# Kernel tuning notes

Measured on AMD Instinct MI355X. Metric: run time of the kernel, lower is better.

The kernel has to match this reference:

```python
import jax, jax.numpy as jnp
import numpy as np

EPS = 1e-06


def rotation_trick(e, q):
    # e, q: (..., D). Faithful to torch version, but r_rT @ e and
    # q_hat_e_hatT @ e are algebraically simplified to r*(r.e) and
    # q_hat*(e_hat.e), avoiding the (..., D, D) outer-product tensors.
    sg = jax.lax.stop_gradient
    e_norm = sg(jnp.linalg.norm(e, axis=-1, keepdims=True)) + EPS
    q_norm = sg(jnp.linalg.norm(q, axis=-1, keepdims=True)) + EPS
    e_hat = sg(e / e_norm)
    q_hat = sg(q / q_norm)
    lmbda = q_norm / e_norm
    r = e_hat + q_hat
    r = r / jnp.linalg.norm(r, axis=-1, keepdims=True)
    r_dot_e = jnp.sum(r * e, axis=-1, keepdims=True)
    ehat_dot_e = jnp.sum(e_hat * e, axis=-1, keepdims=True)
    return lmbda * (e - 2.0 * r * r_dot_e + 2.0 * q_hat * ehat_dot_e)


def setup_inputs() -> dict:
    key = jax.random.key(0)
    k1, k2 = jax.random.split(key)
    B, D, H, W = 8, 64, 32, 32
    K = 8192
    x = jax.random.normal(k1, (B, D, H, W), dtype=jnp.float32)
    # init_tensor: L2-normalize uniform rand along dim=1, scale=1
    e = jax.random.uniform(k2, (D, K), dtype=jnp.float32)
    e_i_ts = e / (jnp.linalg.norm(e, axis=1, keepdims=True) + 1e-12)
    return {"x": x, "e_i_ts": e_i_ts}


def reference(x, e_i_ts):
    # x: (B, D, H, W); e_i_ts: (D, K)
    B, D, H, W = x.shape
    x_perm = jnp.transpose(x, (0, 2, 3, 1))          # (B, H, W, D)
    flat_x = x_perm.reshape(-1, D)                   # (N, D)
    distances = (
        jnp.sum(flat_x**2, axis=1, keepdims=True)
        - 2.0 * flat_x @ e_i_ts
        + jnp.sum(e_i_ts**2, axis=0, keepdims=True)
    )                                                # (N, K)
    encoding_indices = jnp.argmin(distances, axis=1) # (N,)
    ind = encoding_indices.reshape(B, H, W)
    quantized_x = e_i_ts.T[ind]                      # (B, H, W, D) gather
    quantized_x_d = rotation_trick(x_perm, quantized_x)
    # permute back to channels-first
    q = jnp.transpose(quantized_x, (0, 3, 1, 2))
    q_d = jnp.transpose(quantized_x_d, (0, 3, 1, 2))
    return (q_d, q, ind)
```

## Files before the change

### kernel.cpp

```cpp
#include <hip/hip_runtime.h>
#include <float.h>
#include <math.h>

#define EPS 1e-6f

typedef __attribute__((ext_vector_type(8))) short short8;
typedef __attribute__((ext_vector_type(4))) float f32x4;

constexpr int Nn = 8192;
constexpr int Dd = 64;
constexpr int Kk = 8192;
constexpr int PLANE = Nn * Dd;
constexpr int KSPLIT = 16;
constexpr int KPB = Kk / KSPLIT;
constexpr int NT = KPB / 16;
constexpr int NPAIR = NT / 2;
constexpr int TILE_USH = 6 * 64 * 8;
constexpr int TILE_BYTES = TILE_USH * 2;

__device__ __forceinline__ void split3(float v, unsigned short& h1, unsigned short& h2, unsigned short& h3) {
    unsigned u = __float_as_uint(v);
    h1 = (unsigned short)(u >> 16);
    float r1 = v - __uint_as_float((unsigned)h1 << 16);
    h2 = (unsigned short)(__float_as_uint(r1) >> 16);
    float r2 = r1 - __uint_as_float((unsigned)h2 << 16);
    h3 = (unsigned short)(__float_as_uint(r2) >> 16);
}

typedef __attribute__((address_space(3))) unsigned int lds_u32_t;
typedef __attribute__((address_space(1))) unsigned int glb_u32_t;
__device__ __forceinline__ void gload_lds16(const void* g, void* l) {
    __builtin_amdgcn_global_load_lds((const glb_u32_t*)g, (lds_u32_t*)l, 16, 0, 0);
}

__global__ void prep_kernel(const float* __restrict__ e, const float* __restrict__ x,
                            unsigned short* __restrict__ es_t, float* __restrict__ en2h,
                            float* __restrict__ et,
                            unsigned short* __restrict__ xs, float* __restrict__ xn2)
{
    const int tid = threadIdx.x;
    if (blockIdx.x < 32) {
        const int k = blockIdx.x * 256 + tid;
        const int t = k >> 4, l15 = k & 15;
        unsigned short* tb = es_t + (size_t)t * TILE_USH;
        float s = 0.f;
        #pragma unroll
        for (int c = 0; c < 8; ++c) {
            const int ks = c >> 2, kg = c & 3;
            short8 h1v, h2v, h3v;
            float fv[8];
            #pragma unroll
            for (int j = 0; j < 8; ++j) {
                float v = e[(c * 8 + j) * Kk + k];
                fv[j] = v;
                s = fmaf(v, v, s);
                unsigned short h1, h2, h3; split3(v, h1, h2, h3);
                h1v[j] = (short)h1; h2v[j] = (short)h2; h3v[j] = (short)h3;
            }
            const int lofs = (kg * 16 + l15) * 8;
            *(short8*)(tb + (0 * 2 + ks) * 512 + lofs) = h1v;
            *(short8*)(tb + (1 * 2 + ks) * 512 + lofs) = h2v;
            *(short8*)(tb + (2 * 2 + ks) * 512 + lofs) = h3v;
            *(float4*)(et + (size_t)k * Dd + c * 8)     = *(float4*)&fv[0];
            *(float4*)(et + (size_t)k * Dd + c * 8 + 4) = *(float4*)&fv[4];
        }
        en2h[k] = 0.5f * s;
    } else {
        const int p = (blockIdx.x - 32) * 256 + tid;
        const int b = p >> 10, hw = p & 1023;
        float s = 0.f;
        #pragma unroll
        for (int c = 0; c < 8; ++c) {
            short8 h1v, h2v, h3v;
            #pragma unroll
            for (int j = 0; j < 8; ++j) {
                float v = x[(b * Dd + c * 8 + j) * 1024 + hw];
                s = fmaf(v, v, s);
                unsigned short h1, h2, h3; split3(-v, h1, h2, h3);
                h1v[j] = (short)h1; h2v[j] = (short)h2; h3v[j] = (short)h3;
            }
            *(short8*)(xs + (size_t)p * Dd + c * 8) = h1v;
            *(short8*)(xs + PLANE + (size_t)p * Dd + c * 8) = h2v;
            *(short8*)(xs + 2 * PLANE + (size_t)p * Dd + c * 8) = h3v;
        }
        xn2[p] = s;
    }
}

__device__ __forceinline__ void tile_compute(
    const short8 (&a)[2][3][2], const short8 (&b)[6], float en,
    int nb, int l15, float (&bv)[2][4], int (&bi)[2][4])
{
    f32x4 acc[2][2];
    acc[0][0] = f32x4{en, en, en, en}; acc[1][0] = f32x4{en, en, en, en};
    acc[0][1] = f32x4{0.f, 0.f, 0.f, 0.f}; acc[1][1] = f32x4{0.f, 0.f, 0.f, 0.f};
    #define PROD(sx, se) \
        acc[0][0] = __builtin_amdgcn_mfma_f32_16x16x32_bf16(a[0][sx][0], b[(se)*2+0], acc[0][0], 0,0,0); \
        acc[1][0] = __builtin_amdgcn_mfma_f32_16x16x32_bf16(a[1][sx][0], b[(se)*2+0], acc[1][0], 0,0,0); \
        acc[0][1] = __builtin_amdgcn_mfma_f32_16x16x32_bf16(a[0][sx][1], b[(se)*2+1], acc[0][1], 0,0,0); \
        acc[1][1] = __builtin_amdgcn_mfma_f32_16x16x32_bf16(a[1][sx][1], b[(se)*2+1], acc[1][1], 0,0,0);
    PROD(0,0) PROD(0,1) PROD(1,0) PROD(0,2) PROD(1,1) PROD(2,0)
    #undef PROD
    #pragma unroll
    for (int mi = 0; mi < 2; ++mi)
        #pragma unroll
        for (int j = 0; j < 4; ++j) {
            float s = acc[mi][0][j] + acc[mi][1][j];
            if (s < bv[mi][j]) { bv[mi][j] = s; bi[mi][j] = nb + l15; }
        }
}

__global__ __launch_bounds__(256, 2) void dist_mfma(
    const unsigned short* __restrict__ xs, const unsigned short* __restrict__ es_t,
    const float* __restrict__ en2h,
    float* __restrict__ pval, int* __restrict__ pidx)
{
    __shared__ __align__(16) unsigned short sB[2][2 * TILE_USH];

    const int tid = threadIdx.x;
    const int w = tid >> 6, lane = tid & 63;
    const int l15 = lane & 15, kg = lane >> 4;
    const int m0 = blockIdx.x * 128 + w * 32;
    const int t0 = blockIdx.y * NT;

    short8 a[2][3][2];
    #pragma unroll
    for (int mi = 0; mi < 2; ++mi) {
        const unsigned short* xp = xs + (size_t)(m0 + mi * 16 + l15) * Dd + kg * 8;
        #pragma unroll
        for (int s = 0; s < 3; ++s)
            #pragma unroll
            for (int ks = 0; ks < 2; ++ks)
                a[mi][s][ks] = *(const short8*)(xp + s * PLANE + ks * 32);
    }

    float bv[2][4]; int bi[2][4];
    #pragma unroll
    for (int mi = 0; mi < 2; ++mi)
        #pragma unroll
        for (int j = 0; j < 4; ++j) { bv[mi][j] = FLT_MAX; bi[mi][j] = 0; }

    #define STAGE_PAIR(buf, pi) { \
        const char* gb_ = (const char*)es_t + (size_t)(pi) * (2 * TILE_BYTES); \
        char* lb_ = (char*)&sB[buf][0]; \
        _Pragma("unroll") \
        for (int r_ = 0; r_ < 3; ++r_) { \
            const int off_ = r_ * 4096 + w * 1024; \
            gload_lds16(gb_ + off_ + lane * 16, lb_ + off_); } }

    STAGE_PAIR(0, t0 / 2)
    __syncthreads();

    #pragma unroll 1
    for (int p = 0; p < NPAIR; ++p) {
        const int cur = p & 1;
        if (p + 1 < NPAIR) { STAGE_PAIR(cur ^ 1, t0 / 2 + p + 1) }

        const int ti = t0 + p * 2;
        float en0 = en2h[ti * 16 + l15];
        float en1 = en2h[ti * 16 + 16 + l15];

        short8 bf0[6], bf1[6];
        {
            const unsigned short* lb = &sB[cur][lane * 8];
            #pragma unroll
            for (int f = 0; f < 6; ++f) bf0[f] = *(const short8*)(lb + f * 512);
            #pragma unroll
            for (int f = 0; f < 6; ++f) bf1[f] = *(const short8*)(lb + TILE_USH + f * 512);
        }
        tile_compute(a, bf0, en0, ti * 16, l15, bv, bi);
        tile_compute(a, bf1, en1, ti * 16 + 16, l15, bv, bi);

        __syncthreads();
    }

    #pragma unroll
    for (int m = 1; m < 16; m <<= 1) {
        #pragma unroll
        for (int mi = 0; mi < 2; ++mi)
            #pragma unroll
            for (int j = 0; j < 4; ++j) {
                float ov = __shfl_xor(bv[mi][j], m, 64);
                int   oi = __shfl_xor(bi[mi][j], m, 64);
                if (ov < bv[mi][j] || (ov == bv[mi][j] && oi < bi[mi][j])) {
                    bv[mi][j] = ov; bi[mi][j] = oi;
                }
            }
    }
    if (l15 == 0) {
        #pragma unroll
        for (int mi = 0; mi < 2; ++mi)
            #pragma unroll
            for (int j = 0; j < 4; ++j) {
                int pix = m0 + mi * 16 + kg * 4 + j;
                pval[(size_t)pix * KSPLIT + blockIdx.y] = bv[mi][j];
                pidx[(size_t)pix * KSPLIT + blockIdx.y] = bi[mi][j];
            }
    }
}

__global__ __launch_bounds__(256) void finalize_kernel(
    const float* __restrict__ x, const float* __restrict__ et,
    const float* __restrict__ en2h, const float* __restrict__ xn2,
    const float* __restrict__ pval, const int* __restrict__ pidx,
    float* __restrict__ out_qd, float* __restrict__ out_q, float* __restrict__ out_ind)
{
    const int tid = threadIdx.x;
    const int p = blockIdx.x * 256 + tid;

    const float4* pv4 = (const float4*)(pval + (size_t)p * KSPLIT);
    const int4*   pi4 = (const int4*)(pidx + (size_t)p * KSPLIT);
    float bvv = FLT_MAX; int bii = 0;
    #pragma unroll
    for (int u = 0; u < KSPLIT / 4; ++u) {
        float4 v4 = pv4[u]; int4 i4 = pi4[u];
        #pragma unroll
        for (int jj = 0; jj < 4; ++jj) {
            float v = ((const float*)&v4)[jj];
            int   i = ((const int*)&i4)[jj];
            if (v < bvv || (v == bvv && i < bii)) { bvv = v; bii = i; }
        }
    }
    if (blockIdx.y == 0) out_ind[p] = (float)bii;

    float sx2 = xn2[p];
    float enh = en2h[bii];
    float sq2 = 2.f * enh;
    float sxq = enh - bvv;
    float ne = sqrtf(sx2), nq = sqrtf(sq2);
    float inv_e = 1.f / (ne + EPS), inv_q = 1.f / (nq + EPS);
    float lmbda = (nq + EPS) * inv_e;
    float ehat_dot_e = sx2 * inv_e;
    float rn2 = sx2 * inv_e * inv_e + 2.f * sxq * inv_e * inv_q + sq2 * inv_q * inv_q;
    float inv_r = rsqrtf(rn2);
    float rde = (sx2 * inv_e + sxq * inv_q) * inv_r;
    float cx = lmbda * (1.f - 2.f * rde * inv_r * inv_e);
    float cq = 2.f * lmbda * inv_q * (ehat_dot_e - rde * inv_r);

    const int b = p >> 10, hw = p & 1023;
    const int d0 = blockIdx.y * 8;
    const float* xb = x + (b * Dd + d0) * 1024 + hw;
    const float* er = et + (size_t)bii * Dd + d0;
    float* qd_b = out_qd + (b * Dd + d0) * 1024 + hw;
    float* q_b  = out_q  + (b * Dd + d0) * 1024 + hw;
    #pragma unroll
    for (int dv = 0; dv < 2; ++dv) {
        float4 q4 = *(const float4*)(er + dv * 4);
        #pragma unroll
        for (int jj = 0; jj < 4; ++jj) {
            int d = dv * 4 + jj;
            float xv = xb[d * 1024];
            float qv = ((const float*)&q4)[jj];
            qd_b[d * 1024] = cx * xv + cq * qv;
            q_b[d * 1024]  = qv;
        }
    }
}

extern "C" void kernel_launch(void* const* d_in, const int* in_sizes, int n_in,
                              void* d_out, int out_size, void* d_ws, size_t ws_size,
                              hipStream_t stream) {
    const float* x = (const float*)d_in[0];
    const float* e = (const float*)d_in[1];
    float* out = (float*)d_out;
    float* out_qd  = out;
    float* out_q   = out + Nn * Dd;
    float* out_ind = out + 2 * Nn * Dd;

    unsigned short* xs   = (unsigned short*)d_ws;
    unsigned short* es_t = xs + 3 * PLANE;
    float* et   = (float*)(es_t + (size_t)(Kk / 16) * TILE_USH);
    float* en2h = et + (size_t)Kk * Dd;
    float* xn2  = en2h + Kk;
    float* pval = xn2 + Nn;
    int*   pidx = (int*)(pval + (size_t)Nn * KSPLIT);

    prep_kernel<<<64, 256, 0, stream>>>(e, x, es_t, en2h, et, xs, xn2);
    dist_mfma<<<dim3(Nn / 128, KSPLIT), 256, 0, stream>>>(xs, es_t, en2h, pval, pidx);
    finalize_kernel<<<dim3(32, 8), 256, 0, stream>>>(x, et, en2h, xn2, pval, pidx,
                                                     out_qd, out_q, out_ind);
}
```

Before: 64.29 us.

## Software-pipeline codebook LDS staging with explicit vmcnt waits and ping-pong unroll

Restructures the distance kernel's main loop into an unrolled two-stage ping-pong over the two LDS buffers. The next tile pair is staged, along with its norm values, before the current pair is computed. Explicit s_waitcnt vmcnt(5) and raw s_barrier calls replace __syncthreads, so only the older loads are waited on and the prefetch overlaps the MFMA work. The en2h loads are also hoisted one stage ahead. In exchange, the code relies on exact counting of outstanding memory ops and on hand-placed scheduling barriers, and the final iterations issue a redundant clamped prefetch.

```diff
diff --git a/kernel.cpp b/kernel.cpp
--- a/kernel.cpp
+++ b/kernel.cpp
@@ -122,6 +122,7 @@
     const int l15 = lane & 15, kg = lane >> 4;
     const int m0 = blockIdx.x * 128 + w * 32;
     const int t0 = blockIdx.y * NT;
+    const int pr0 = t0 / 2;
 
     short8 a[2][3][2];
     #pragma unroll
@@ -148,30 +149,53 @@
             const int off_ = r_ * 4096 + w * 1024; \
             gload_lds16(gb_ + off_ + lane * 16, lb_ + off_); } }
 
-    STAGE_PAIR(0, t0 / 2)
-    __syncthreads();
+    #define COMPUTE_PAIR(buf, pp_, e0_, e1_) { \
+        const int ti_ = t0 + (pp_) * 2; \
+        short8 bf0[6], bf1[6]; \
+        const unsigned short* lb = &sB[buf][lane * 8]; \
+        _Pragma("unroll") \
+        for (int f = 0; f < 6; ++f) bf0[f] = *(const short8*)(lb + f * 512); \
+        _Pragma("unroll") \
+        for (int f = 0; f < 6; ++f) bf1[f] = *(const short8*)(lb + TILE_USH + f * 512); \
+        tile_compute(a, bf0, e0_, ti_ * 16, l15, bv, bi); \
+        tile_compute(a, bf1, e1_, ti_ * 16 + 16, l15, bv, bi); }
+
+    STAGE_PAIR(0, pr0)
+    float enA0 = en2h[t0 * 16 + l15];
+    float enA1 = en2h[t0 * 16 + 16 + l15];
+    float enB0, enB1;
+    asm volatile("s_waitcnt vmcnt(0)" ::: "memory");
+    __builtin_amdgcn_s_barrier();
+    __builtin_amdgcn_sched_barrier(0);
 
     #pragma unroll 1
-    for (int p = 0; p < NPAIR; ++p) {
-        const int cur = p & 1;
-        if (p + 1 < NPAIR) { STAGE_PAIR(cur ^ 1, t0 / 2 + p + 1) }
-
-        const int ti = t0 + p * 2;
-        float en0 = en2h[ti * 16 + l15];
-        float en1 = en2h[ti * 16 + 16 + l15];
-
-        short8 bf0[6], bf1[6];
+    for (int pp = 0; pp < NPAIR; pp += 2) {
         {
-            const unsigned short* lb = &sB[cur][lane * 8];
-            #pragma unroll
-            for (int f = 0; f < 6; ++f) bf0[f] = *(const short8*)(lb + f * 512);
-            #pragma unroll
-            for (int f = 0; f < 6; ++f) bf1[f] = *(const short8*)(lb + TILE_USH + f * 512);
-        }
-        tile_compute(a, bf0, en0, ti * 16, l15, bv, bi);
-        tile_compute(a, bf1, en1, ti * 16 + 16, l15, bv, bi);
-
-        __syncthreads();
+            const int pn = (pp + 1 < NPAIR) ? pp + 1 : NPAIR - 1;
+            STAGE_PAIR(1, pr0 + pn)
+            enB0 = en2h[(t0 + 2 * pn) * 16 + l15];
+            enB1 = en2h[(t0 + 2 * pn) * 16 + 16 + l15];
+            asm volatile("s_waitcnt vmcnt(5)" ::: "memory");
+            __builtin_amdgcn_sched_barrier(0);
+            __builtin_amdgcn_s_barrier();
+            __builtin_amdgcn_sched_barrier(0);
+            COMPUTE_PAIR(0, pp, enA0, enA1)
+            __builtin_amdgcn_sched_barrier(0);
+            __builtin_amdgcn_s_barrier();
+        }
+        {
+            const int pn = (pp + 2 < NPAIR) ? pp + 2 : NPAIR - 1;
+            STAGE_PAIR(0, pr0 + pn)
+            enA0 = en2h[(t0 + 2 * pn) * 16 + l15];
+            enA1 = en2h[(t0 + 2 * pn) * 16 + 16 + l15];
+            asm volatile("s_waitcnt vmcnt(5)" ::: "memory");
+            __builtin_amdgcn_sched_barrier(0);
+            __builtin_amdgcn_s_barrier();
+            __builtin_amdgcn_sched_barrier(0);
+            COMPUTE_PAIR(1, pp + 1, enB0, enB1)
+            __builtin_amdgcn_sched_barrier(0);
+            __builtin_amdgcn_s_barrier();
+        }
     }
 
     #pragma unroll
```

Result: slower. 66.93 us (+4.1%).

## Fold codeword norms into staged tiles via MFMA and restructure LDS pipeline barriers

Applied to the files above, without the earlier changes.

The half squared norm of each codeword is now split into three bf16 parts and stored as a seventh fragment in each staged tile. A ones-vector MFMA adds it into the accumulator, which removes the per-iteration global loads of en2h. The double-buffered LDS loop now uses explicit s_waitcnt/s_barrier asm: it issues the next prefetch unconditionally, waits only on the older loads, and puts a barrier after the fragment reads instead of at the end of the loop. This adds one MFMA and more LDS traffic per tile, and relies on the hand-written waitcnt counts being correct.

```diff
diff --git a/kernel.cpp b/kernel.cpp
--- a/kernel.cpp
+++ b/kernel.cpp
@@ -15,8 +15,8 @@
 constexpr int KPB = Kk / KSPLIT;
 constexpr int NT = KPB / 16;
 constexpr int NPAIR = NT / 2;
-constexpr int TILE_USH = 6 * 64 * 8;
-constexpr int TILE_BYTES = TILE_USH * 2;
+constexpr int TILE_USH = 4096;
+constexpr int PAIR_BYTES = 2 * TILE_USH * 2;
 
 __device__ __forceinline__ void split3(float v, unsigned short& h1, unsigned short& h2, unsigned short& h3) {
     unsigned u = __float_as_uint(v);
@@ -64,6 +64,13 @@
             *(float4*)(et + (size_t)k * Dd + c * 8)     = *(float4*)&fv[0];
             *(float4*)(et + (size_t)k * Dd + c * 8 + 4) = *(float4*)&fv[4];
         }
+        unsigned short s1, s2, s3; split3(0.5f * s, s1, s2, s3);
+        short8 env = {(short)s1, (short)s2, (short)s3, 0, 0, 0, 0, 0};
+        short8 zz  = {0, 0, 0, 0, 0, 0, 0, 0};
+        *(short8*)(tb + 6 * 512 + l15 * 8) = env;
+        *(short8*)(tb + 6 * 512 + (16 + l15) * 8) = zz;
+        *(short8*)(tb + 6 * 512 + (32 + l15) * 8) = zz;
+        *(short8*)(tb + 6 * 512 + (48 + l15) * 8) = zz;
         en2h[k] = 0.5f * s;
     } else {
         const int p = (blockIdx.x - 32) * 256 + tid;
@@ -88,12 +95,14 @@
 }
 
 __device__ __forceinline__ void tile_compute(
-    const short8 (&a)[2][3][2], const short8 (&b)[6], float en,
+    const short8 (&a)[2][3][2], const short8 a_ones, const short8 (&b)[7],
     int nb, int l15, float (&bv)[2][4], int (&bi)[2][4])
 {
+    const f32x4 zero = {0.f, 0.f, 0.f, 0.f};
+    f32x4 acc_en = __builtin_amdgcn_mfma_f32_16x16x32_bf16(a_ones, b[6], zero, 0, 0, 0);
     f32x4 acc[2][2];
-    acc[0][0] = f32x4{en, en, en, en}; acc[1][0] = f32x4{en, en, en, en};
-    acc[0][1] = f32x4{0.f, 0.f, 0.f, 0.f}; acc[1][1] = f32x4{0.f, 0.f, 0.f, 0.f};
+    acc[0][0] = acc_en; acc[1][0] = acc_en;
+    acc[0][1] = zero;   acc[1][1] = zero;
     #define PROD(sx, se) \
         acc[0][0] = __builtin_amdgcn_mfma_f32_16x16x32_bf16(a[0][sx][0], b[(se)*2+0], acc[0][0], 0,0,0); \
         acc[1][0] = __builtin_amdgcn_mfma_f32_16x16x32_bf16(a[1][sx][0], b[(se)*2+0], acc[1][0], 0,0,0); \
@@ -112,7 +121,6 @@
 
 __global__ __launch_bounds__(256, 2) void dist_mfma(
     const unsigned short* __restrict__ xs, const unsigned short* __restrict__ es_t,
-    const float* __restrict__ en2h,
     float* __restrict__ pval, int* __restrict__ pidx)
 {
     __shared__ __align__(16) unsigned short sB[2][2 * TILE_USH];
@@ -122,6 +130,7 @@
     const int l15 = lane & 15, kg = lane >> 4;
     const int m0 = blockIdx.x * 128 + w * 32;
     const int t0 = blockIdx.y * NT;
+    const int pr0 = t0 / 2;
 
     short8 a[2][3][2];
     #pragma unroll
@@ -133,6 +142,9 @@
             for (int ks = 0; ks < 2; ++ks)
                 a[mi][s][ks] = *(const short8*)(xp + s * PLANE + ks * 32);
     }
+    const short8 a_ones = (kg == 0)
+        ? short8{(short)0x3F80, (short)0x3F80, (short)0x3F80, 0, 0, 0, 0, 0}
+        : short8{0, 0, 0, 0, 0, 0, 0, 0};
 
     float bv[2][4]; int bi[2][4];
     #pragma unroll
@@ -141,37 +153,37 @@
         for (int j = 0; j < 4; ++j) { bv[mi][j] = FLT_MAX; bi[mi][j] = 0; }
 
     #define STAGE_PAIR(buf, pi) { \
-        const char* gb_ = (const char*)es_t + (size_t)(pi) * (2 * TILE_BYTES); \
+        const char* gb_ = (const char*)es_t + (size_t)(pi) * PAIR_BYTES; \
         char* lb_ = (char*)&sB[buf][0]; \
         _Pragma("unroll") \
-        for (int r_ = 0; r_ < 3; ++r_) { \
+        for (int r_ = 0; r_ < 4; ++r_) { \
             const int off_ = r_ * 4096 + w * 1024; \
             gload_lds16(gb_ + off_ + lane * 16, lb_ + off_); } }
 
-    STAGE_PAIR(0, t0 / 2)
-    __syncthreads();
+    STAGE_PAIR(0, pr0)
+    asm volatile("s_waitcnt vmcnt(0)" ::: "memory");
+    asm volatile("s_barrier" ::: "memory");
 
     #pragma unroll 1
-    for (int p = 0; p < NPAIR; ++p) {
-        const int cur = p & 1;
-        if (p + 1 < NPAIR) { STAGE_PAIR(cur ^ 1, t0 / 2 + p + 1) }
-
-        const int ti = t0 + p * 2;
-        float en0 = en2h[ti * 16 + l15];
-        float en1 = en2h[ti * 16 + 16 + l15];
-
-        short8 bf0[6], bf1[6];
-        {
-            const unsigned short* lb = &sB[cur][lane * 8];
-            #pragma unroll
-            for (int f = 0; f < 6; ++f) bf0[f] = *(const short8*)(lb + f * 512);
-            #pragma unroll
-            for (int f = 0; f < 6; ++f) bf1[f] = *(const short8*)(lb + TILE_USH + f * 512);
-        }
-        tile_compute(a, bf0, en0, ti * 16, l15, bv, bi);
-        tile_compute(a, bf1, en1, ti * 16 + 16, l15, bv, bi);
-
-        __syncthreads();
+    for (int pp = 0; pp < NPAIR; ++pp) {
+        const int cur = pp & 1;
+        const int pn = (pp + 1 < NPAIR) ? pp + 1 : NPAIR - 1;
+        STAGE_PAIR(cur ^ 1, pr0 + pn)
+        asm volatile("s_waitcnt vmcnt(4)" ::: "memory");
+        asm volatile("s_barrier" ::: "memory");
+
+        short8 bf0[7], bf1[7];
+        const unsigned short* lb = &sB[cur][lane * 8];
+        #pragma unroll
+        for (int f = 0; f < 7; ++f) bf0[f] = *(const short8*)(lb + f * 512);
+        #pragma unroll
+        for (int f = 0; f < 7; ++f) bf1[f] = *(const short8*)(lb + TILE_USH + f * 512);
+        asm volatile("s_waitcnt lgkmcnt(0)" ::: "memory");
+        asm volatile("s_barrier" ::: "memory");
+
+        const int ti = t0 + pp * 2;
+        tile_compute(a, a_ones, bf0, ti * 16, l15, bv, bi);
+        tile_compute(a, a_ones, bf1, ti * 16 + 16, l15, bv, bi);
     }
 
     #pragma unroll
@@ -276,7 +288,7 @@
     int*   pidx = (int*)(pval + (size_t)Nn * KSPLIT);
 
     prep_kernel<<<64, 256, 0, stream>>>(e, x, es_t, en2h, et, xs, xn2);
-    dist_mfma<<<dim3(Nn / 128, KSPLIT), 256, 0, stream>>>(xs, es_t, en2h, pval, pidx);
+    dist_mfma<<<dim3(Nn / 128, KSPLIT), 256, 0, stream>>>(xs, es_t, pval, pidx);
     finalize_kernel<<<dim3(32, 8), 256, 0, stream>>>(x, et, en2h, xn2, pval, pidx,
                                                      out_qd, out_q, out_ind);
 }
```

Result: no change. 65.44 us (+1.8%).

## Switch distance GEMM to 32x32x16 MFMA with explicit waitcnt double buffering

Applied to the files above, without the earlier changes.

Replaces the 16x16x32 bf16 MFMA tiles with 32x32x16 MFMAs, repacking the codebook tiles in the prep kernel so each LDS tile holds 32 codewords. Each wave now covers 32 pixels by 32 codewords per tile with fewer instructions and less operand traffic per FLOP. The pipeline uses manual s_waitcnt/s_barrier double buffering and setprio around the MFMA block instead of __syncthreads, and the argmin reduction now spans 32 lanes. This costs more accumulator registers and relies on the hand-written wait counts being correct.

```diff
diff --git a/kernel.cpp b/kernel.cpp
--- a/kernel.cpp
+++ b/kernel.cpp
@@ -6,6 +6,7 @@
 
 typedef __attribute__((ext_vector_type(8))) short short8;
 typedef __attribute__((ext_vector_type(4))) float f32x4;
+typedef __attribute__((ext_vector_type(16))) float f32x16;
 
 constexpr int Nn = 8192;
 constexpr int Dd = 64;
@@ -13,9 +14,8 @@
 constexpr int PLANE = Nn * Dd;
 constexpr int KSPLIT = 16;
 constexpr int KPB = Kk / KSPLIT;
-constexpr int NT = KPB / 16;
-constexpr int NPAIR = NT / 2;
-constexpr int TILE_USH = 6 * 64 * 8;
+constexpr int NTILE = KPB / 32;
+constexpr int TILE_USH = 12 * 512;
 constexpr int TILE_BYTES = TILE_USH * 2;
 
 __device__ __forceinline__ void split3(float v, unsigned short& h1, unsigned short& h2, unsigned short& h3) {
@@ -41,12 +41,12 @@
     const int tid = threadIdx.x;
     if (blockIdx.x < 32) {
         const int k = blockIdx.x * 256 + tid;
-        const int t = k >> 4, l15 = k & 15;
+        const int t = k >> 5, cwin = k & 31;
         unsigned short* tb = es_t + (size_t)t * TILE_USH;
         float s = 0.f;
         #pragma unroll
         for (int c = 0; c < 8; ++c) {
-            const int ks = c >> 2, kg = c & 3;
+            const int q = c >> 1, half = c & 1;
             short8 h1v, h2v, h3v;
             float fv[8];
             #pragma unroll
@@ -57,10 +57,10 @@
                 unsigned short h1, h2, h3; split3(v, h1, h2, h3);
                 h1v[j] = (short)h1; h2v[j] = (short)h2; h3v[j] = (short)h3;
             }
-            const int lofs = (kg * 16 + l15) * 8;
-            *(short8*)(tb + (0 * 2 + ks) * 512 + lofs) = h1v;
-            *(short8*)(tb + (1 * 2 + ks) * 512 + lofs) = h2v;
-            *(short8*)(tb + (2 * 2 + ks) * 512 + lofs) = h3v;
+            const int lofs = (cwin + 32 * half) * 8;
+            *(short8*)(tb + (0 * 4 + q) * 512 + lofs) = h1v;
+            *(short8*)(tb + (1 * 4 + q) * 512 + lofs) = h2v;
+            *(short8*)(tb + (2 * 4 + q) * 512 + lofs) = h3v;
             *(float4*)(et + (size_t)k * Dd + c * 8)     = *(float4*)&fv[0];
             *(float4*)(et + (size_t)k * Dd + c * 8 + 4) = *(float4*)&fv[4];
         }
@@ -87,27 +87,28 @@
     }
 }
 
-__device__ __forceinline__ void tile_compute(
-    const short8 (&a)[2][3][2], const short8 (&b)[6], float en,
-    int nb, int l15, float (&bv)[2][4], int (&bi)[2][4])
-{
-    f32x4 acc[2][2];
-    acc[0][0] = f32x4{en, en, en, en}; acc[1][0] = f32x4{en, en, en, en};
-    acc[0][1] = f32x4{0.f, 0.f, 0.f, 0.f}; acc[1][1] = f32x4{0.f, 0.f, 0.f, 0.f};
-    #define PROD(sx, se) \
-        acc[0][0] = __builtin_amdgcn_mfma_f32_16x16x32_bf16(a[0][sx][0], b[(se)*2+0], acc[0][0], 0,0,0); \
-        acc[1][0] = __builtin_amdgcn_mfma_f32_16x16x32_bf16(a[1][sx][0], b[(se)*2+0], acc[1][0], 0,0,0); \
-        acc[0][1] = __builtin_amdgcn_mfma_f32_16x16x32_bf16(a[0][sx][1], b[(se)*2+1], acc[0][1], 0,0,0); \
-        acc[1][1] = __builtin_amdgcn_mfma_f32_16x16x32_bf16(a[1][sx][1], b[(se)*2+1], acc[1][1], 0,0,0);
-    PROD(0,0) PROD(0,1) PROD(1,0) PROD(0,2) PROD(1,1) PROD(2,0)
-    #undef PROD
-    #pragma unroll
-    for (int mi = 0; mi < 2; ++mi)
-        #pragma unroll
-        for (int j = 0; j < 4; ++j) {
-            float s = acc[mi][0][j] + acc[mi][1][j];
-            if (s < bv[mi][j]) { bv[mi][j] = s; bi[mi][j] = nb + l15; }
-        }
+__device__ __forceinline__ void tile_compute32(
+    const short8 (&a)[3][4], const short8 (&b)[12], float en,
+    int cw, float (&bv)[16], int (&bi)[16])
+{
+    f32x16 acc0, acc1;
+    #pragma unroll
+    for (int r = 0; r < 16; ++r) { acc0[r] = en; acc1[r] = 0.f; }
+    #define PRODQ(q) { \
+        f32x16& ac = ((q) & 1) ? acc1 : acc0; \
+        ac = __builtin_amdgcn_mfma_f32_32x32x16_bf16(a[0][q], b[0 * 4 + (q)], ac, 0,0,0); \
+        ac = __builtin_amdgcn_mfma_f32_32x32x16_bf16(a[0][q], b[1 * 4 + (q)], ac, 0,0,0); \
+        ac = __builtin_amdgcn_mfma_f32_32x32x16_bf16(a[1][q], b[0 * 4 + (q)], ac, 0,0,0); \
+        ac = __builtin_amdgcn_mfma_f32_32x32x16_bf16(a[0][q], b[2 * 4 + (q)], ac, 0,0,0); \
+        ac = __builtin_amdgcn_mfma_f32_32x32x16_bf16(a[1][q], b[1 * 4 + (q)], ac, 0,0,0); \
+        ac = __builtin_amdgcn_mfma_f32_32x32x16_bf16(a[2][q], b[0 * 4 + (q)], ac, 0,0,0); }
+    PRODQ(0) PRODQ(1) PRODQ(2) PRODQ(3)
+    #undef PRODQ
+    #pragma unroll
+    for (int r = 0; r < 16; ++r) {
+        float v = acc0[r] + acc1[r];
+        if (v < bv[r]) { bv[r] = v; bi[r] = cw; }
+    }
 }
 
 __global__ __launch_bounds__(256, 2) void dist_mfma(
@@ -115,87 +116,93 @@
     const float* __restrict__ en2h,
     float* __restrict__ pval, int* __restrict__ pidx)
 {
-    __shared__ __align__(16) unsigned short sB[2][2 * TILE_USH];
+    __shared__ __align__(16) unsigned short sB[2][TILE_USH];
 
     const int tid = threadIdx.x;
     const int w = tid >> 6, lane = tid & 63;
-    const int l15 = lane & 15, kg = lane >> 4;
+    const int col = lane & 31, half = lane >> 5;
     const int m0 = blockIdx.x * 128 + w * 32;
-    const int t0 = blockIdx.y * NT;
-
-    short8 a[2][3][2];
-    #pragma unroll
-    for (int mi = 0; mi < 2; ++mi) {
-        const unsigned short* xp = xs + (size_t)(m0 + mi * 16 + l15) * Dd + kg * 8;
-        #pragma unroll
-        for (int s = 0; s < 3; ++s)
-            #pragma unroll
-            for (int ks = 0; ks < 2; ++ks)
-                a[mi][s][ks] = *(const short8*)(xp + s * PLANE + ks * 32);
-    }
-
-    float bv[2][4]; int bi[2][4];
-    #pragma unroll
-    for (int mi = 0; mi < 2; ++mi)
-        #pragma unroll
-        for (int j = 0; j < 4; ++j) { bv[mi][j] = FLT_MAX; bi[mi][j] = 0; }
-
-    #define STAGE_PAIR(buf, pi) { \
-        const char* gb_ = (const char*)es_t + (size_t)(pi) * (2 * TILE_BYTES); \
+    const int tg0 = blockIdx.y * NTILE;
+    const int k0 = blockIdx.y * KPB;
+
+    short8 a[3][4];
+    #pragma unroll
+    for (int s = 0; s < 3; ++s)
+        #pragma unroll
+        for (int q = 0; q < 4; ++q)
+            a[s][q] = *(const short8*)(xs + (size_t)(m0 + col) * Dd + s * PLANE + q * 16 + 8 * half);
+
+    float bv[16]; int bi[16];
+    #pragma unroll
+    for (int r = 0; r < 16; ++r) { bv[r] = FLT_MAX; bi[r] = 0; }
+
+    #define STAGE_TILE(buf, ti) { \
+        const char* gb_ = (const char*)es_t + (size_t)(tg0 + (ti)) * TILE_BYTES; \
         char* lb_ = (char*)&sB[buf][0]; \
         _Pragma("unroll") \
         for (int r_ = 0; r_ < 3; ++r_) { \
             const int off_ = r_ * 4096 + w * 1024; \
             gload_lds16(gb_ + off_ + lane * 16, lb_ + off_); } }
 
-    STAGE_PAIR(0, t0 / 2)
-    __syncthreads();
+    #define DSREAD(bf, buf) { \
+        const unsigned short* lb = &sB[buf][lane * 8]; \
+        _Pragma("unroll") \
+        for (int f = 0; f < 12; ++f) bf[f] = *(const short8*)(lb + f * 512); }
+
+    STAGE_TILE(0, 0)
+    float enA = en2h[k0 + col];
+    float enB;
+    asm volatile("s_waitcnt vmcnt(0)" ::: "memory");
+    asm volatile("s_barrier" ::: "memory");
 
     #pragma unroll 1
-    for (int p = 0; p < NPAIR; ++p) {
-        const int cur = p & 1;
-        if (p + 1 < NPAIR) { STAGE_PAIR(cur ^ 1, t0 / 2 + p + 1) }
-
-        const int ti = t0 + p * 2;
-        float en0 = en2h[ti * 16 + l15];
-        float en1 = en2h[ti * 16 + 16 + l15];
-
-        short8 bf0[6], bf1[6];
+    for (int tt = 0; tt < NTILE; tt += 2) {
         {
-            const unsigned short* lb = &sB[cur][lane * 8];
-            #pragma unroll
-            for (int f = 0; f < 6; ++f) bf0[f] = *(const short8*)(lb + f * 512);
-            #pragma unroll
-            for (int f = 0; f < 6; ++f) bf1[f] = *(const short8*)(lb + TILE_USH + f * 512);
-        }
-        tile_compute(a, bf0, en0, ti * 16, l15, bv, bi);
-        tile_compute(a, bf1, en1, ti * 16 + 16, l15, bv, bi);
-
-        __syncthreads();
-    }
-
-    #pragma unroll
-    for (int m = 1; m < 16; m <<= 1) {
-        #pragma unroll
-        for (int mi = 0; mi < 2; ++mi)
-            #pragma unroll
-            for (int j = 0; j < 4; ++j) {
-                float ov = __shfl_xor(bv[mi][j], m, 64);
-                int   oi = __shfl_xor(bi[mi][j], m, 64);
-                if (ov < bv[mi][j] || (ov == bv[mi][j] && oi < bi[mi][j])) {
-                    bv[mi][j] = ov; bi[mi][j] = oi;
-                }
-            }
-    }
-    if (l15 == 0) {
-        #pragma unroll
-        for (int mi = 0; mi < 2; ++mi)
-            #pragma unroll
-            for (int j = 0; j < 4; ++j) {
-                int pix = m0 + mi * 16 + kg * 4 + j;
-                pval[(size_t)pix * KSPLIT + blockIdx.y] = bv[mi][j];
-                pidx[(size_t)pix * KSPLIT + blockIdx.y] = bi[mi][j];
-            }
+            const int pn = (tt + 1 < NTILE) ? tt + 1 : NTILE - 1;
+            STAGE_TILE(1, pn)
+            enB = en2h[k0 + pn * 32 + col];
+            asm volatile("s_waitcnt vmcnt(4)" ::: "memory");
+            asm volatile("s_barrier" ::: "memory");
+            short8 bf[12];
+            DSREAD(bf, 0)
+            asm volatile("s_waitcnt lgkmcnt(0)" ::: "memory");
+            asm volatile("s_barrier" ::: "memory");
+            __builtin_amdgcn_s_setprio(1);
+            tile_compute32(a, bf, enA, k0 + tt * 32 + col, bv, bi);
+            __builtin_amdgcn_s_setprio(0);
+        }
+        {
+            const int pn = (tt + 2 < NTILE) ? tt + 2 : NTILE - 1;
+            STAGE_TILE(0, pn)
+            enA = en2h[k0 + pn * 32 + col];
+            asm volatile("s_waitcnt vmcnt(4)" ::: "memory");
+            asm volatile("s_barrier" ::: "memory");
+            short8 bf[12];
+            DSREAD(bf, 1)
+            asm volatile("s_waitcnt lgkmcnt(0)" ::: "memory");
+            asm volatile("s_barrier" ::: "memory");
+            __builtin_amdgcn_s_setprio(1);
+            tile_compute32(a, bf, enB, k0 + (tt + 1) * 32 + col, bv, bi);
+            __builtin_amdgcn_s_setprio(0);
+        }
+    }
+
+    #pragma unroll
+    for (int m = 1; m < 32; m <<= 1) {
+        #pragma unroll
+        for (int r = 0; r < 16; ++r) {
+            float ov = __shfl_xor(bv[r], m, 64);
+            int   oi = __shfl_xor(bi[r], m, 64);
+            if (ov < bv[r] || (ov == bv[r] && oi < bi[r])) { bv[r] = ov; bi[r] = oi; }
+        }
+    }
+    if (col == 0) {
+        #pragma unroll
+        for (int r = 0; r < 16; ++r) {
+            int pix = m0 + (r & 3) + 8 * (r >> 2) + 4 * half;
+            pval[(size_t)pix * KSPLIT + blockIdx.y] = bv[r];
+            pidx[(size_t)pix * KSPLIT + blockIdx.y] = bi[r];
+        }
     }
 }
 
@@ -269,7 +276,7 @@
 
     unsigned short* xs   = (unsigned short*)d_ws;
     unsigned short* es_t = xs + 3 * PLANE;
-    float* et   = (float*)(es_t + (size_t)(Kk / 16) * TILE_USH);
+    float* et   = (float*)(es_t + (size_t)(Kk / 32) * TILE_USH);
     float* en2h = et + (size_t)Kk * Dd;
     float* xn2  = en2h + Kk;
     float* pval = xn2 + Nn;
```

Measured after the change: 80.21 us. +24.8%, slower.
